# Kernel tuning notes

Measured on AMD Instinct MI355X. Metric: run time of the kernel, lower is better.

## Reference

```python
import jax, jax.numpy as jnp
import numpy as np

EMBED = 1024
HEADS = 16
HEAD_DIM = EMBED // HEADS


def setup_inputs() -> dict:
    key = jax.random.key(0)
    ks = jax.random.split(key, 9)
    B, S = 1, 4096
    scale = 1.0 / np.sqrt(EMBED)
    x = jax.random.normal(ks[0], (B, S, EMBED), dtype=jnp.float32)
    # nn.Linear weights stored as [out, in]; we store transposed [in, out] for x @ W
    Wq = jax.random.uniform(ks[1], (EMBED, EMBED), jnp.float32, -scale, scale)
    bq = jax.random.uniform(ks[2], (EMBED,), jnp.float32, -scale, scale)
    Wk = jax.random.uniform(ks[3], (EMBED, EMBED), jnp.float32, -scale, scale)
    bk = jax.random.uniform(ks[4], (EMBED,), jnp.float32, -scale, scale)
    Wv = jax.random.uniform(ks[5], (EMBED, EMBED), jnp.float32, -scale, scale)
    bv = jax.random.uniform(ks[6], (EMBED,), jnp.float32, -scale, scale)
    Wo = jax.random.uniform(ks[7], (EMBED, EMBED), jnp.float32, -scale, scale)
    bo = jax.random.uniform(ks[8], (EMBED,), jnp.float32, -scale, scale)
    return {"x": x, "Wq": Wq, "bq": bq, "Wk": Wk, "bk": bk,
            "Wv": Wv, "bv": bv, "Wo": Wo, "bo": bo}


def reference(x, Wq, bq, Wk, bk, Wv, bv, Wo, bo):
    B, S, E = x.shape
    H, D = HEADS, HEAD_DIM
    # projections
    Q = (x @ Wq + bq).reshape(B, S, H, D).transpose(0, 2, 1, 3)  # [B,H,S,D]
    K = (x @ Wk + bk).reshape(B, S, H, D).transpose(0, 2, 1, 3)
    V = (x @ Wv + bv).reshape(B, S, H, D).transpose(0, 2, 1, 3)
    # unfused attention: full [B,H,S,S] score matrix, matching the torch module
    scores = jnp.einsum('bhqd,bhkd->bhqk', Q, K) / jnp.sqrt(jnp.float32(D)).astype(x.dtype)
    probs = jax.nn.softmax(scores, axis=-1)
    out = jnp.einsum('bhqk,bhkd->bhqd', probs, V)  # [B,H,S,D]
    out = out.transpose(0, 2, 1, 3).reshape(B, S, E)
    return out @ Wo + bo
```

## Files before the change

kernel.cpp:

```cpp
#include <hip/hip_runtime.h>


constexpr int Sq = 4096;
constexpr int Ee = 1024;
constexpr int Hh = 16;
constexpr int Dh = 64;

typedef _Float16 half8 __attribute__((ext_vector_type(8)));
typedef _Float16 half4 __attribute__((ext_vector_type(4)));
typedef _Float16 half2t __attribute__((ext_vector_type(2)));
typedef float f32x4 __attribute__((ext_vector_type(4)));

union U8 { half8 v8; half2t h2[4]; };

__device__ __forceinline__ unsigned short f2h(float f) {
  _Float16 h = (_Float16)f;
  return *reinterpret_cast<unsigned short*>(&h);
}

__device__ __forceinline__ half2t pk(float a, float b) {
  return __builtin_bit_cast(half2t, __builtin_amdgcn_cvt_pkrtz(a, b));
}

__device__ __forceinline__ void gload16(const void* g, void* l) {
  __builtin_amdgcn_global_load_lds(
      (const __attribute__((address_space(1))) void*)g,
      (__attribute__((address_space(3))) void*)l, 16, 0, 0);
}

__global__ void k_prep(const float* __restrict__ x,
                       const float* __restrict__ Wq, const float* __restrict__ Wk,
                       const float* __restrict__ Wv, const float* __restrict__ Wo,
                       unsigned short* __restrict__ xb,
                       unsigned short* __restrict__ Wqt, unsigned short* __restrict__ Wkt,
                       unsigned short* __restrict__ Wvt, unsigned short* __restrict__ Wot) {
  int b = blockIdx.x, t = threadIdx.x;
  if (b < 4096) {
    int i = b * 256 + t;
    float4 v = reinterpret_cast<const float4*>(x)[i];
    ushort4 o;
    o.x = f2h(v.x); o.y = f2h(v.y); o.z = f2h(v.z); o.w = f2h(v.w);
    reinterpret_cast<ushort4*>(xb)[i] = o;
    return;
  }
  __shared__ unsigned short tile[64][65];
  int r = b - 4096;
  int wi = r >> 8, ti = r & 255;
  const float* W = (wi == 0) ? Wq : (wi == 1) ? Wk : (wi == 2) ? Wv : Wo;
  unsigned short* Wt = (wi == 0) ? Wqt : (wi == 1) ? Wkt : (wi == 2) ? Wvt : Wot;
  int kb = (ti & 15) * 64, nb = (ti >> 4) * 64;
  int r0 = t >> 4, c4 = (t & 15) * 4;
  for (int i = 0; i < 4; i++) {
    int row = r0 + i * 16;
    float4 v = *reinterpret_cast<const float4*>(W + (size_t)(kb + row) * Ee + nb + c4);
    tile[row][c4 + 0] = f2h(v.x); tile[row][c4 + 1] = f2h(v.y);
    tile[row][c4 + 2] = f2h(v.z); tile[row][c4 + 3] = f2h(v.w);
  }
  __syncthreads();
  for (int i = 0; i < 4; i++) {
    int nrow = r0 + i * 16;
    ushort4 o;
    o.x = tile[c4 + 0][nrow]; o.y = tile[c4 + 1][nrow];
    o.z = tile[c4 + 2][nrow]; o.w = tile[c4 + 3][nrow];
    *reinterpret_cast<ushort4*>(Wt + (size_t)(nb + nrow) * Ee + kb + c4) = o;
  }
}

template <bool TR>
__device__ __forceinline__ void gemm_kloop(
    const unsigned short* __restrict__ A, const unsigned short* __restrict__ Wt,
    unsigned short* Al, unsigned short* Bl,
    int m0, int n0, int t, int wm, int wn, int quad, int c, f32x4 (&acc)[4][4]) {
  auto stageAB = [&](int buf, int k0) {
#pragma unroll
    for (int i = 0; i < 4; i++) {
      int ch = i * 256 + t;
      int row = ch >> 3, kg = (ch & 7) ^ (row & 7);
      gload16(A + (size_t)(m0 + row) * 1024 + k0 + kg * 8, &Al[buf * 8192 + ch * 8]);
    }
#pragma unroll
    for (int i = 0; i < 4; i++) {
      int ch = i * 256 + t;
      int row = ch >> 3, kg = (ch & 7) ^ (row & 7);
      gload16(Wt + (size_t)(n0 + row) * 1024 + k0 + kg * 8, &Bl[buf * 8192 + ch * 8]);
    }
  };
  stageAB(0, 0);
  __syncthreads();
  for (int k0 = 0; k0 < 1024; k0 += 64) {
    int cur = (k0 >> 6) & 1;
    if (k0 < 960) stageAB(cur ^ 1, k0 + 64);
    const unsigned short* Ab = &Al[cur * 8192];
    const unsigned short* Bb = &Bl[cur * 8192];
#pragma unroll
    for (int ks = 0; ks < 2; ks++) {
      half8 af[4], bfr[4];
#pragma unroll
      for (int i = 0; i < 4; i++) {
        int row = wm * 64 + i * 16 + c;
        int kg = (quad + 4 * ks) ^ (row & 7);
        af[i] = *reinterpret_cast<const half8*>(&Ab[row * 64 + kg * 8]);
      }
#pragma unroll
      for (int j = 0; j < 4; j++) {
        int row = wn * 64 + j * 16 + c;
        int kg = (quad + 4 * ks) ^ (row & 7);
        bfr[j] = *reinterpret_cast<const half8*>(&Bb[row * 64 + kg * 8]);
      }
#pragma unroll
      for (int i = 0; i < 4; i++)
#pragma unroll
        for (int j = 0; j < 4; j++) {
          if (TR)
            acc[j][i] = __builtin_amdgcn_mfma_f32_16x16x32_f16(bfr[j], af[i], acc[j][i], 0, 0, 0);
          else
            acc[i][j] = __builtin_amdgcn_mfma_f32_16x16x32_f16(af[i], bfr[j], acc[i][j], 0, 0, 0);
        }
    }
    __syncthreads();
  }
}

__global__ __launch_bounds__(256) void k_gemm(
    const unsigned short* __restrict__ A,
    const unsigned short* __restrict__ W0, const unsigned short* __restrict__ W1,
    const unsigned short* __restrict__ W2,
    const float* __restrict__ b0, const float* __restrict__ b1, const float* __restrict__ b2,
    void* d0, void* d1, void* d2) {
  __shared__ __align__(16) unsigned short Al[2 * 128 * 64];
  __shared__ __align__(16) unsigned short Bl[2 * 128 * 64];
  const unsigned short* Wt; const float* bias; void* dst;
  if (blockIdx.z == 0)      { Wt = W0; bias = b0; dst = d0; }
  else if (blockIdx.z == 1) { Wt = W1; bias = b1; dst = d1; }
  else                      { Wt = W2; bias = b2; dst = d2; }

  int t = threadIdx.x;
  int w = t >> 6, L = t & 63, quad = L >> 4, c = L & 15;
  int m0 = blockIdx.x * 128, n0 = blockIdx.y * 128;
  int wm = w >> 1, wn = w & 1;

  f32x4 zero = {0.f, 0.f, 0.f, 0.f};
  f32x4 acc[4][4];
#pragma unroll
  for (int i = 0; i < 4; i++)
#pragma unroll
    for (int j = 0; j < 4; j++) acc[i][j] = zero;

  if (blockIdx.z < 2) gemm_kloop<true>(A, Wt, Al, Bl, m0, n0, t, wm, wn, quad, c, acc);
  else                gemm_kloop<false>(A, Wt, Al, Bl, m0, n0, t, wm, wn, quad, c, acc);

  if (blockIdx.z < 2) {
    float sc = (blockIdx.z == 0) ? 0.18033688011112042f : 1.0f;
    unsigned short* qk = (unsigned short*)dst;
#pragma unroll
    for (int j = 0; j < 4; j++) {
      int nb4 = n0 + wn * 64 + j * 16 + quad * 4;
      int hh = nb4 >> 6, d = nb4 & 63;
      f32x4 b4 = *reinterpret_cast<const f32x4*>(bias + nb4);
#pragma unroll
      for (int i = 0; i < 4; i++) {
        int s = m0 + wm * 64 + i * 16 + c;
        half4 hv;
#pragma unroll
        for (int r = 0; r < 4; r++) hv[r] = (_Float16)((acc[j][i][r] + b4[r]) * sc);
        *reinterpret_cast<half4*>(&qk[(size_t)hh * Sq * Dh + (size_t)s * Dh + d]) = hv;
      }
    }
    return;
  }
  unsigned short* Vt = (unsigned short*)dst;
#pragma unroll
  for (int j = 0; j < 4; j++) {
    int n = n0 + wn * 64 + j * 16 + c;
    int hh = n >> 6, d = n & 63;
    float bv = bias[n];
#pragma unroll
    for (int i = 0; i < 4; i++) {
      int pos = m0 + wm * 64 + (i >> 1) * 32 + quad * 8 + (i & 1) * 4;
      half4 hv;
#pragma unroll
      for (int r = 0; r < 4; r++) hv[r] = (_Float16)(acc[i][j][r] + bv);
      *reinterpret_cast<half4*>(&Vt[(size_t)hh * Dh * Sq + (size_t)d * Sq + pos]) = hv;
    }
  }
}

__global__ __launch_bounds__(256) void k_gemmO(
    const unsigned short* __restrict__ A, const unsigned short* __restrict__ Wt,
    const float* __restrict__ bias, float* __restrict__ out) {
  __shared__ __align__(16) unsigned short Al[2 * 64 * 64];
  __shared__ __align__(16) unsigned short Bl[2 * 128 * 64];
  int t = threadIdx.x;
  int w = t >> 6, L = t & 63, quad = L >> 4, c = L & 15;
  int m0 = blockIdx.x * 64, n0 = blockIdx.y * 128;
  int wm = w & 1, wn = w >> 1;

  f32x4 zero = {0.f, 0.f, 0.f, 0.f};
  f32x4 acc[4][2];
#pragma unroll
  for (int j = 0; j < 4; j++)
#pragma unroll
    for (int i = 0; i < 2; i++) acc[j][i] = zero;

  auto stageAB = [&](int buf, int k0) {
#pragma unroll
    for (int i = 0; i < 2; i++) {
      int ch = i * 256 + t;
      int row = ch >> 3, kg = (ch & 7) ^ (row & 7);
      gload16(A + (size_t)(m0 + row) * 1024 + k0 + kg * 8, &Al[buf * 4096 + ch * 8]);
    }
#pragma unroll
    for (int i = 0; i < 4; i++) {
      int ch = i * 256 + t;
      int row = ch >> 3, kg = (ch & 7) ^ (row & 7);
      gload16(Wt + (size_t)(n0 + row) * 1024 + k0 + kg * 8, &Bl[buf * 8192 + ch * 8]);
    }
  };
  stageAB(0, 0);
  __syncthreads();
  for (int k0 = 0; k0 < 1024; k0 += 64) {
    int cur = (k0 >> 6) & 1;
    if (k0 < 960) stageAB(cur ^ 1, k0 + 64);
    const unsigned short* Ab = &Al[cur * 4096];
    const unsigned short* Bb = &Bl[cur * 8192];
#pragma unroll
    for (int ks = 0; ks < 2; ks++) {
      half8 af[2], bfr[4];
#pragma unroll
      for (int i = 0; i < 2; i++) {
        int row = wm * 32 + i * 16 + c;
        int kg = (quad + 4 * ks) ^ (row & 7);
        af[i] = *reinterpret_cast<const half8*>(&Ab[row * 64 + kg * 8]);
      }
#pragma unroll
      for (int j = 0; j < 4; j++) {
        int row = wn * 64 + j * 16 + c;
        int kg = (quad + 4 * ks) ^ (row & 7);
        bfr[j] = *reinterpret_cast<const half8*>(&Bb[row * 64 + kg * 8]);
      }
#pragma unroll
      for (int j = 0; j < 4; j++)
#pragma unroll
        for (int i = 0; i < 2; i++)
          acc[j][i] = __builtin_amdgcn_mfma_f32_16x16x32_f16(bfr[j], af[i], acc[j][i], 0, 0, 0);
    }
    __syncthreads();
  }

#pragma unroll
  for (int j = 0; j < 4; j++) {
    int nb4 = n0 + wn * 64 + j * 16 + quad * 4;
    f32x4 b4 = *reinterpret_cast<const f32x4*>(bias + nb4);
#pragma unroll
    for (int i = 0; i < 2; i++) {
      int s = m0 + wm * 32 + i * 16 + c;
      f32x4 v = acc[j][i] + b4;
      *reinterpret_cast<f32x4*>(out + (size_t)s * 1024 + nb4) = v;
    }
  }
}

__global__ __launch_bounds__(256, 2) void k_attn(
    const unsigned short* __restrict__ Q, const unsigned short* __restrict__ K,
    const unsigned short* __restrict__ Vt, unsigned short* __restrict__ O) {
  __shared__ __align__(16) unsigned short SM[32768];
  int t = threadIdx.x;
  int w = t >> 6, L = t & 63, quad = L >> 4, c = L & 15;
  int wl = w & 1, par = w >> 1;
  int h = blockIdx.y, qb = blockIdx.x;
  const unsigned short* Qh = Q + (size_t)h * Sq * Dh;
  const unsigned short* Kh = K + (size_t)h * Sq * Dh;
  const unsigned short* Vth = Vt + (size_t)h * Dh * Sq;

  half8 qf[4][2];
#pragma unroll
  for (int qg = 0; qg < 4; qg++) {
    int qrow = qb * 128 + wl * 64 + qg * 16 + c;
#pragma unroll
    for (int ks = 0; ks < 2; ks++)
      qf[qg][ks] = *reinterpret_cast<const half8*>(Qh + (size_t)qrow * Dh + ks * 32 + quad * 8);
  }

  f32x4 zero = {0.f, 0.f, 0.f, 0.f};
  f32x4 o[4][4];
  f32x4 l[4];
#pragma unroll
  for (int qg = 0; qg < 4; qg++) {
    l[qg] = zero;
#pragma unroll
    for (int dt = 0; dt < 4; dt++) o[qg][dt] = zero;
  }
  half8 ones8;
#pragma unroll
  for (int j = 0; j < 8; j++) ones8[j] = (_Float16)1.0f;

  int koff[2][4], voff[4][2];
#pragma unroll
  for (int ks = 0; ks < 2; ks++)
#pragma unroll
    for (int nt = 0; nt < 4; nt++) {
      int row = nt * 16 + c;
      koff[ks][nt] = par * 4096 + row * 64 + (((ks * 4 + quad) ^ (row & 7)) * 8);
    }
#pragma unroll
  for (int dt = 0; dt < 4; dt++)
#pragma unroll
    for (int n2 = 0; n2 < 2; n2++) {
      int row = dt * 16 + c;
      voff[dt][n2] = (2 + par) * 4096 + row * 64 + (((n2 * 4 + quad) ^ (row & 7)) * 8);
    }

  const unsigned short* KgB[2];
  const unsigned short* VgB[2];
#pragma unroll
  for (int i = 0; i < 2; i++) {
    int ch = i * 256 + t;
    int row = ch >> 3, kg = (ch & 7) ^ (row & 7);
    KgB[i] = Kh + row * Dh + kg * 8;
    VgB[i] = Vth + (size_t)row * Sq + kg * 8;
  }

  auto stage = [&](int bufo, int tb) {
#pragma unroll
    for (int p2 = 0; p2 < 2; p2++) {
#pragma unroll
      for (int i = 0; i < 2; i++)
        gload16(KgB[i] + (size_t)(tb + p2) * 4096, &SM[bufo + p2 * 4096 + (i * 256 + t) * 8]);
#pragma unroll
      for (int i = 0; i < 2; i++)
        gload16(VgB[i] + (size_t)(tb + p2) * 64, &SM[bufo + (2 + p2) * 4096 + (i * 256 + t) * 8]);
    }
  };

  stage(0, 0);

  auto body = [&](int BUFOFF) {
    half8 pB[4][2];
#pragma unroll
    for (int h2 = 0; h2 < 2; h2++) {
      f32x4 st[2][4];
      __builtin_amdgcn_s_setprio(1);
#pragma unroll
      for (int nt = 0; nt < 4; nt++) {
        half8 kfv = *reinterpret_cast<const half8*>(&SM[koff[0][nt] + BUFOFF]);
        st[0][nt] = __builtin_amdgcn_mfma_f32_16x16x32_f16(kfv, qf[2 * h2 + 0][0], zero, 0, 0, 0);
        st[1][nt] = __builtin_amdgcn_mfma_f32_16x16x32_f16(kfv, qf[2 * h2 + 1][0], zero, 0, 0, 0);
      }
#pragma unroll
      for (int nt = 0; nt < 4; nt++) {
        half8 kfv = *reinterpret_cast<const half8*>(&SM[koff[1][nt] + BUFOFF]);
        st[0][nt] = __builtin_amdgcn_mfma_f32_16x16x32_f16(kfv, qf[2 * h2 + 0][1], st[0][nt], 0, 0, 0);
        st[1][nt] = __builtin_amdgcn_mfma_f32_16x16x32_f16(kfv, qf[2 * h2 + 1][1], st[1][nt], 0, 0, 0);
      }
      __builtin_amdgcn_s_setprio(0);
#pragma unroll
      for (int q2 = 0; q2 < 2; q2++)
#pragma unroll
        for (int n2 = 0; n2 < 2; n2++) {
          U8 u;
          u.h2[0] = pk(__builtin_amdgcn_exp2f(st[q2][2 * n2][0]), __builtin_amdgcn_exp2f(st[q2][2 * n2][1]));
          u.h2[1] = pk(__builtin_amdgcn_exp2f(st[q2][2 * n2][2]), __builtin_amdgcn_exp2f(st[q2][2 * n2][3]));
          u.h2[2] = pk(__builtin_amdgcn_exp2f(st[q2][2 * n2 + 1][0]), __builtin_amdgcn_exp2f(st[q2][2 * n2 + 1][1]));
          u.h2[3] = pk(__builtin_amdgcn_exp2f(st[q2][2 * n2 + 1][2]), __builtin_amdgcn_exp2f(st[q2][2 * n2 + 1][3]));
          pB[2 * h2 + q2][n2] = u.v8;
          l[2 * h2 + q2] = __builtin_amdgcn_mfma_f32_16x16x32_f16(ones8, u.v8, l[2 * h2 + q2], 0, 0, 0);
        }
    }
    __builtin_amdgcn_s_setprio(1);
#pragma unroll
    for (int dt = 0; dt < 4; dt++)
#pragma unroll
      for (int n2 = 0; n2 < 2; n2++) {
        half8 vv = *reinterpret_cast<const half8*>(&SM[voff[dt][n2] + BUFOFF]);
        o[0][dt] = __builtin_amdgcn_mfma_f32_16x16x32_f16(vv, pB[0][n2], o[0][dt], 0, 0, 0);
        o[1][dt] = __builtin_amdgcn_mfma_f32_16x16x32_f16(vv, pB[1][n2], o[1][dt], 0, 0, 0);
        o[2][dt] = __builtin_amdgcn_mfma_f32_16x16x32_f16(vv, pB[2][n2], o[2][dt], 0, 0, 0);
        o[3][dt] = __builtin_amdgcn_mfma_f32_16x16x32_f16(vv, pB[3][n2], o[3][dt], 0, 0, 0);
      }
    __builtin_amdgcn_s_setprio(0);
  };

  for (int ob2 = 0; ob2 < 16; ob2++) {
    __syncthreads();
    stage(16384, 4 * ob2 + 2);
    body(0);
    __syncthreads();
    if (ob2 < 15) stage(0, 4 * ob2 + 4);
    body(16384);
  }

  __syncthreads();
  float* cb = (float*)SM;
  if (par == 1) {
#pragma unroll
    for (int qg = 0; qg < 4; qg++)
#pragma unroll
      for (int dt = 0; dt < 4; dt++)
        *reinterpret_cast<f32x4*>(cb + ((wl * 17 + qg * 4 + dt) * 64 + L) * 4) = o[qg][dt];
    f32x4 lv = {l[0][0], l[1][0], l[2][0], l[3][0]};
    *reinterpret_cast<f32x4*>(cb + ((wl * 17 + 16) * 64 + L) * 4) = lv;
  }
  __syncthreads();
  if (par == 0) {
#pragma unroll
    for (int qg = 0; qg < 4; qg++)
#pragma unroll
      for (int dt = 0; dt < 4; dt++)
        o[qg][dt] += *reinterpret_cast<const f32x4*>(cb + ((wl * 17 + qg * 4 + dt) * 64 + L) * 4);
    f32x4 lv = *reinterpret_cast<const f32x4*>(cb + ((wl * 17 + 16) * 64 + L) * 4);
#pragma unroll
    for (int qg = 0; qg < 4; qg++) {
      float inv = 1.f / (l[qg][0] + lv[qg]);
      int q = qb * 128 + wl * 64 + qg * 16 + c;
#pragma unroll
      for (int dt = 0; dt < 4; dt++) {
        half4 hv;
#pragma unroll
        for (int r = 0; r < 4; r++) hv[r] = (_Float16)(o[qg][dt][r] * inv);
        *reinterpret_cast<half4*>(&O[(size_t)q * 1024 + h * 64 + dt * 16 + quad * 4]) = hv;
      }
    }
  }
}

extern "C" void kernel_launch(void* const* d_in, const int* in_sizes, int n_in,
                              void* d_out, int out_size, void* d_ws, size_t ws_size,
                              hipStream_t stream) {
  const float* x  = (const float*)d_in[0];
  const float* Wq = (const float*)d_in[1];
  const float* bq = (const float*)d_in[2];
  const float* Wk = (const float*)d_in[3];
  const float* bk = (const float*)d_in[4];
  const float* Wv = (const float*)d_in[5];
  const float* bv = (const float*)d_in[6];
  const float* Wo = (const float*)d_in[7];
  const float* bo = (const float*)d_in[8];

  char* ws = (char*)d_ws;
  const size_t MB = 1u << 20;
  unsigned short* xb  = (unsigned short*)(ws);
  unsigned short* Wqt = (unsigned short*)(ws + 8 * MB);
  unsigned short* Wkt = (unsigned short*)(ws + 10 * MB);
  unsigned short* Wvt = (unsigned short*)(ws + 12 * MB);
  unsigned short* Wot = (unsigned short*)(ws + 14 * MB);
  unsigned short* Qb  = (unsigned short*)(ws + 16 * MB);
  unsigned short* Kb  = (unsigned short*)(ws + 24 * MB);
  unsigned short* Vtg = (unsigned short*)(ws + 32 * MB);
  unsigned short* Ob  = (unsigned short*)(ws + 40 * MB);

  k_prep<<<5120, 256, 0, stream>>>(x, Wq, Wk, Wv, Wo, xb, Wqt, Wkt, Wvt, Wot);
  k_gemm<<<dim3(32, 8, 3), 256, 0, stream>>>(xb, Wqt, Wkt, Wvt, bq, bk, bv,
                                             (void*)Qb, (void*)Kb, (void*)Vtg);
  k_attn<<<dim3(32, 16), 256, 0, stream>>>(Qb, Kb, Vtg, Ob);
  k_gemmO<<<dim3(64, 8), 256, 0, stream>>>(Ob, Wot, bo, (float*)d_out);
}
```

Measured before the change: 216.0 us.

## Prefetch two K-tiles ahead with vmcnt waits and remap GEMM block order

Both projection GEMMs now issue loads for two K-tiles before computing. Each iteration waits with a partial s_waitcnt vmcnt and raw s_barrier, so the next tile's global-to-LDS loads overlap the MFMA work instead of draining fully every step. The grids are flattened to 1D, with the N-tile index varying fastest, so consecutive blocks share A rows and hit L2 better. This relies on exact vmcnt counting and buffer reuse, which is fragile if the load count per stage changes.

```diff
diff --git a/kernel.cpp b/kernel.cpp
--- a/kernel.cpp
+++ b/kernel.cpp
@@ -85,11 +85,7 @@
       gload16(Wt + (size_t)(n0 + row) * 1024 + k0 + kg * 8, &Bl[buf * 8192 + ch * 8]);
     }
   };
-  stageAB(0, 0);
-  __syncthreads();
-  for (int k0 = 0; k0 < 1024; k0 += 64) {
-    int cur = (k0 >> 6) & 1;
-    if (k0 < 960) stageAB(cur ^ 1, k0 + 64);
+  auto compute = [&](int cur) {
     const unsigned short* Ab = &Al[cur * 8192];
     const unsigned short* Bb = &Bl[cur * 8192];
 #pragma unroll
@@ -117,8 +113,22 @@
             acc[i][j] = __builtin_amdgcn_mfma_f32_16x16x32_f16(af[i], bfr[j], acc[i][j], 0, 0, 0);
         }
     }
-    __syncthreads();
-  }
+  };
+  stageAB(0, 0);
+  stageAB(1, 64);
+  for (int k0 = 0; k0 < 960; k0 += 64) {
+    int cur = (k0 >> 6) & 1;
+    asm volatile("s_waitcnt vmcnt(8)" ::: "memory");
+    __builtin_amdgcn_s_barrier();
+    __builtin_amdgcn_sched_barrier(0);
+    compute(cur);
+    __builtin_amdgcn_s_barrier();
+    if (k0 < 896) stageAB(cur, k0 + 128);
+  }
+  asm volatile("s_waitcnt vmcnt(0)" ::: "memory");
+  __builtin_amdgcn_s_barrier();
+  __builtin_amdgcn_sched_barrier(0);
+  compute(1);
 }
 
 __global__ __launch_bounds__(256) void k_gemm(
@@ -129,14 +139,19 @@
     void* d0, void* d1, void* d2) {
   __shared__ __align__(16) unsigned short Al[2 * 128 * 64];
   __shared__ __align__(16) unsigned short Bl[2 * 128 * 64];
+  int bid = blockIdx.x;
+  int yp = bid & 7;
+  int rest = bid >> 3;
+  int xm = rest & 31;
+  int z = rest >> 5;
   const unsigned short* Wt; const float* bias; void* dst;
-  if (blockIdx.z == 0)      { Wt = W0; bias = b0; dst = d0; }
-  else if (blockIdx.z == 1) { Wt = W1; bias = b1; dst = d1; }
-  else                      { Wt = W2; bias = b2; dst = d2; }
+  if (z == 0)      { Wt = W0; bias = b0; dst = d0; }
+  else if (z == 1) { Wt = W1; bias = b1; dst = d1; }
+  else             { Wt = W2; bias = b2; dst = d2; }
 
   int t = threadIdx.x;
   int w = t >> 6, L = t & 63, quad = L >> 4, c = L & 15;
-  int m0 = blockIdx.x * 128, n0 = blockIdx.y * 128;
+  int m0 = xm * 128, n0 = yp * 128;
   int wm = w >> 1, wn = w & 1;
 
   f32x4 zero = {0.f, 0.f, 0.f, 0.f};
@@ -146,11 +161,11 @@
 #pragma unroll
     for (int j = 0; j < 4; j++) acc[i][j] = zero;
 
-  if (blockIdx.z < 2) gemm_kloop<true>(A, Wt, Al, Bl, m0, n0, t, wm, wn, quad, c, acc);
-  else                gemm_kloop<false>(A, Wt, Al, Bl, m0, n0, t, wm, wn, quad, c, acc);
-
-  if (blockIdx.z < 2) {
-    float sc = (blockIdx.z == 0) ? 0.18033688011112042f : 1.0f;
+  if (z < 2) gemm_kloop<true>(A, Wt, Al, Bl, m0, n0, t, wm, wn, quad, c, acc);
+  else       gemm_kloop<false>(A, Wt, Al, Bl, m0, n0, t, wm, wn, quad, c, acc);
+
+  if (z < 2) {
+    float sc = (z == 0) ? 0.18033688011112042f : 1.0f;
     unsigned short* qk = (unsigned short*)dst;
 #pragma unroll
     for (int j = 0; j < 4; j++) {
@@ -190,9 +205,12 @@
     const float* __restrict__ bias, float* __restrict__ out) {
   __shared__ __align__(16) unsigned short Al[2 * 64 * 64];
   __shared__ __align__(16) unsigned short Bl[2 * 128 * 64];
+  int bid = blockIdx.x;
+  int yp = bid & 7;
+  int xm = bid >> 3;
   int t = threadIdx.x;
   int w = t >> 6, L = t & 63, quad = L >> 4, c = L & 15;
-  int m0 = blockIdx.x * 64, n0 = blockIdx.y * 128;
+  int m0 = xm * 64, n0 = yp * 128;
   int wm = w & 1, wn = w >> 1;
 
   f32x4 zero = {0.f, 0.f, 0.f, 0.f};
@@ -216,11 +234,7 @@
       gload16(Wt + (size_t)(n0 + row) * 1024 + k0 + kg * 8, &Bl[buf * 8192 + ch * 8]);
     }
   };
-  stageAB(0, 0);
-  __syncthreads();
-  for (int k0 = 0; k0 < 1024; k0 += 64) {
-    int cur = (k0 >> 6) & 1;
-    if (k0 < 960) stageAB(cur ^ 1, k0 + 64);
+  auto compute = [&](int cur) {
     const unsigned short* Ab = &Al[cur * 4096];
     const unsigned short* Bb = &Bl[cur * 8192];
 #pragma unroll
@@ -244,8 +258,22 @@
         for (int i = 0; i < 2; i++)
           acc[j][i] = __builtin_amdgcn_mfma_f32_16x16x32_f16(bfr[j], af[i], acc[j][i], 0, 0, 0);
     }
-    __syncthreads();
-  }
+  };
+  stageAB(0, 0);
+  stageAB(1, 64);
+  for (int k0 = 0; k0 < 960; k0 += 64) {
+    int cur = (k0 >> 6) & 1;
+    asm volatile("s_waitcnt vmcnt(6)" ::: "memory");
+    __builtin_amdgcn_s_barrier();
+    __builtin_amdgcn_sched_barrier(0);
+    compute(cur);
+    __builtin_amdgcn_s_barrier();
+    if (k0 < 896) stageAB(cur, k0 + 128);
+  }
+  asm volatile("s_waitcnt vmcnt(0)" ::: "memory");
+  __builtin_amdgcn_s_barrier();
+  __builtin_amdgcn_sched_barrier(0);
+  compute(1);
 
 #pragma unroll
   for (int j = 0; j < 4; j++) {
@@ -449,8 +477,8 @@
   unsigned short* Ob  = (unsigned short*)(ws + 40 * MB);
 
   k_prep<<<5120, 256, 0, stream>>>(x, Wq, Wk, Wv, Wo, xb, Wqt, Wkt, Wvt, Wot);
-  k_gemm<<<dim3(32, 8, 3), 256, 0, stream>>>(xb, Wqt, Wkt, Wvt, bq, bk, bv,
-                                             (void*)Qb, (void*)Kb, (void*)Vtg);
+  k_gemm<<<768, 256, 0, stream>>>(xb, Wqt, Wkt, Wvt, bq, bk, bv,
+                                  (void*)Qb, (void*)Kb, (void*)Vtg);
   k_attn<<<dim3(32, 16), 256, 0, stream>>>(Qb, Kb, Vtg, Ob);
-  k_gemmO<<<dim3(64, 8), 256, 0, stream>>>(Ob, Wot, bo, (float*)d_out);
-}
+  k_gemmO<<<512, 256, 0, stream>>>(Ob, Wot, bo, (float*)d_out);
+}
```

After: 220.9 us. +2.3%, slower.
